# Optimization experiments

Hardware: AMD Instinct MI355X
Metric: run time of the kernel (lower is better)

Reference implementation:

```python
import jax, jax.numpy as jnp
import numpy as np

N, E = 50000, 800000
IN_DIM, HEADS, OUT_DIM = 256, 8, 32
NEG_SLOPE = 0.2  # PyG GATConv default leaky_relu slope
LN_EPS = 1e-5


def setup_inputs() -> dict:
    key = jax.random.key(0)
    ks = jax.random.split(key, 8)
    HC = HEADS * OUT_DIM
    x = jax.random.normal(ks[0], (N, IN_DIM), dtype=jnp.float32)
    edge_index = jax.random.randint(ks[1], (2, E), 0, N, dtype=jnp.int32)
    # GATConv params: lin (no bias), att_src/att_dst [H,C], output bias [H*C]
    W = jax.random.normal(ks[2], (IN_DIM, HC), dtype=jnp.float32) / np.sqrt(IN_DIM)
    att_src = jax.random.normal(ks[3], (HEADS, OUT_DIM), dtype=jnp.float32) / np.sqrt(OUT_DIM)
    att_dst = jax.random.normal(ks[4], (HEADS, OUT_DIM), dtype=jnp.float32) / np.sqrt(OUT_DIM)
    bias = jnp.zeros((HC,), dtype=jnp.float32)
    ln_gamma = jnp.ones((HC,), dtype=jnp.float32)
    ln_beta = jnp.zeros((HC,), dtype=jnp.float32)
    return {"x": x, "edge_index": edge_index, "W": W, "att_src": att_src,
            "att_dst": att_dst, "bias": bias, "ln_gamma": ln_gamma, "ln_beta": ln_beta}


def reference(x, edge_index, W, att_src, att_dst, bias, ln_gamma, ln_beta):
    n = x.shape[0]
    # GATConv adds self-loops by default
    loop = jnp.arange(n, dtype=edge_index.dtype)
    src = jnp.concatenate([edge_index[0], loop])  # [E+N]
    dst = jnp.concatenate([edge_index[1], loop])
    h = (x @ W).reshape(n, HEADS, OUT_DIM)              # [N,H,C]
    a_src = jnp.einsum('nhc,hc->nh', h, att_src)        # [N,H]
    a_dst = jnp.einsum('nhc,hc->nh', h, att_dst)
    e = jax.nn.leaky_relu(a_src[src] + a_dst[dst], NEG_SLOPE)  # [E+N,H]
    # segment-softmax over incoming edges of each destination node
    m = jax.ops.segment_max(e, dst, num_segments=n)
    e = jnp.exp(e - m[dst])
    denom = jax.ops.segment_sum(e, dst, num_segments=n)
    alpha = e / (denom[dst] + 1e-16)                    # [E+N,H]
    out = jax.ops.segment_sum(h[src] * alpha[:, :, None], dst, num_segments=n)
    out = out.reshape(n, HEADS * OUT_DIM) + bias        # concat heads + bias
    # LayerNorm(out_dim*heads); dropout is identity in eval
    mu = jnp.mean(out, axis=-1, keepdims=True)
    var = jnp.mean(jnp.square(out - mu), axis=-1, keepdims=True)
    return ln_gamma * (out - mu) * jax.lax.rsqrt(var + LN_EPS) + ln_beta
```

## Files before the change

### kernel.cpp

```cpp
#include <hip/hip_runtime.h>

#define HEADS 8
#define OUT_DIM 32
#define HC 256
#define IN_DIM 256
#define NEG_SLOPE 0.2f
#define LN_EPS 1e-5f
#define CAP 64

typedef __attribute__((ext_vector_type(8))) short bf16x8;
typedef __attribute__((ext_vector_type(4))) float f32x4;

__device__ __forceinline__ unsigned short f2bf(float f) {
    unsigned int u = __float_as_uint(f);
    unsigned int r = u + 0x7FFFu + ((u >> 16) & 1u);
    return (unsigned short)(r >> 16);
}
__device__ __forceinline__ float bf2f(unsigned short u) {
    return __uint_as_float((unsigned int)u << 16);
}

__global__ __launch_bounds__(256) void cast_wT(const float* __restrict__ W,
                                               unsigned short* __restrict__ Wt) {
    __shared__ float tile[64][65];
    const int n0 = (blockIdx.x & 3) * 64;
    const int k0 = (blockIdx.x >> 2) * 64;
    const int t = threadIdx.x;
    const int r = t >> 4;
    const int c = (t & 15) * 4;
#pragma unroll
    for (int j = 0; j < 4; j++) {
        const int kl = r + j * 16;
        const float4 v = *(const float4*)(W + (size_t)(k0 + kl) * HC + n0 + c);
        tile[kl][c + 0] = v.x; tile[kl][c + 1] = v.y;
        tile[kl][c + 2] = v.z; tile[kl][c + 3] = v.w;
    }
    __syncthreads();
#pragma unroll
    for (int j = 0; j < 4; j++) {
        const int nr = r + j * 16;
        ushort4 o;
        o.x = f2bf(tile[c + 0][nr]);
        o.y = f2bf(tile[c + 1][nr]);
        o.z = f2bf(tile[c + 2][nr]);
        o.w = f2bf(tile[c + 3][nr]);
        *(ushort4*)(Wt + (size_t)(n0 + nr) * IN_DIM + k0 + c) = o;
    }
}

__global__ __launch_bounds__(256) void gemm_bf16(const float* __restrict__ X,
                                                 const unsigned short* __restrict__ Wt,
                                                 unsigned short* __restrict__ Hb,
                                                 const float* __restrict__ att_s,
                                                 const float* __restrict__ att_d,
                                                 float* __restrict__ a_s,
                                                 float* __restrict__ a_d, int M) {
    __shared__ unsigned short smem[128 * 40 + 256 * 40];
    unsigned short* As = smem;
    unsigned short* Bs = smem + 128 * 40;
    const int t = threadIdx.x;
    const int m0 = blockIdx.x * 128;
    const int w = t >> 6, lane = t & 63;
    const int wr = w >> 1, wn = w & 1;
    const int l16 = lane & 15, quad = lane >> 4;

    f32x4 acc[4][8] = {};

    for (int k0 = 0; k0 < IN_DIM; k0 += 32) {
#pragma unroll
        for (int j = 0; j < 4; j++) {
            const int idx = t + j * 256;
            const int row = idx >> 3;
            const int part = idx & 7;
            float4 v = make_float4(0.f, 0.f, 0.f, 0.f);
            const int gm = m0 + row;
            if (gm < M) v = *(const float4*)(X + (size_t)gm * IN_DIM + k0 + part * 4);
            ushort4 b;
            b.x = f2bf(v.x); b.y = f2bf(v.y); b.z = f2bf(v.z); b.w = f2bf(v.w);
            *(ushort4*)&As[row * 40 + part * 4] = b;
        }
#pragma unroll
        for (int j = 0; j < 4; j++) {
            const int idx = t + j * 256;
            const int n = idx >> 2;
            const int part = idx & 3;
            *(uint4*)&Bs[n * 40 + part * 8] =
                *(const uint4*)(Wt + (size_t)n * IN_DIM + k0 + part * 8);
        }
        __syncthreads();

        bf16x8 af[4];
#pragma unroll
        for (int mi = 0; mi < 4; mi++) {
            const int row = wr * 64 + mi * 16 + l16;
            af[mi] = *(const bf16x8*)&As[row * 40 + quad * 8];
        }
#pragma unroll
        for (int ni = 0; ni < 8; ni++) {
            const int col = wn * 128 + ni * 16 + l16;
            const bf16x8 bfr = *(const bf16x8*)&Bs[col * 40 + quad * 8];
#pragma unroll
            for (int mi = 0; mi < 4; mi++)
                acc[mi][ni] = __builtin_amdgcn_mfma_f32_16x16x32_bf16(af[mi], bfr, acc[mi][ni], 0, 0, 0);
        }
        __syncthreads();
    }

    {
        float as_v[8], ad_v[8];
#pragma unroll
        for (int ni = 0; ni < 8; ni++) {
            as_v[ni] = att_s[wn * 128 + ni * 16 + l16];
            ad_v[ni] = att_d[wn * 128 + ni * 16 + l16];
        }
#pragma unroll
        for (int mi = 0; mi < 4; mi++) {
#pragma unroll
            for (int reg = 0; reg < 4; reg++) {
                float ps0 = acc[mi][0][reg] * as_v[0] + acc[mi][1][reg] * as_v[1];
                float ps1 = acc[mi][2][reg] * as_v[2] + acc[mi][3][reg] * as_v[3];
                float ps2 = acc[mi][4][reg] * as_v[4] + acc[mi][5][reg] * as_v[5];
                float ps3 = acc[mi][6][reg] * as_v[6] + acc[mi][7][reg] * as_v[7];
                float pd0 = acc[mi][0][reg] * ad_v[0] + acc[mi][1][reg] * ad_v[1];
                float pd1 = acc[mi][2][reg] * ad_v[2] + acc[mi][3][reg] * ad_v[3];
                float pd2 = acc[mi][4][reg] * ad_v[4] + acc[mi][5][reg] * ad_v[5];
                float pd3 = acc[mi][6][reg] * ad_v[6] + acc[mi][7][reg] * ad_v[7];
#pragma unroll
                for (int m = 1; m <= 2; m <<= 1) {
                    ps0 += __shfl_xor(ps0, m); ps1 += __shfl_xor(ps1, m);
                    ps2 += __shfl_xor(ps2, m); ps3 += __shfl_xor(ps3, m);
                    pd0 += __shfl_xor(pd0, m); pd1 += __shfl_xor(pd1, m);
                    pd2 += __shfl_xor(pd2, m); pd3 += __shfl_xor(pd3, m);
                }
                const int s2 = l16 & 3;
                float vs = s2 == 0 ? ps0 : (s2 == 1 ? ps1 : (s2 == 2 ? ps2 : ps3));
                float vd = s2 == 0 ? pd0 : (s2 == 1 ? pd1 : (s2 == 2 ? pd2 : pd3));
                vs += __shfl_xor(vs, 4); vs += __shfl_xor(vs, 8);
                vd += __shfl_xor(vd, 4); vd += __shfl_xor(vd, 8);
                const int gm = m0 + wr * 64 + mi * 16 + quad * 4 + reg;
                if (l16 < 4 && gm < M) {
                    a_s[(size_t)gm * HEADS + wn * 4 + l16] = vs;
                    a_d[(size_t)gm * HEADS + wn * 4 + l16] = vd;
                }
            }
        }
    }

    unsigned short* cbuf = smem + w * 2048;
#pragma unroll
    for (int mi = 0; mi < 4; mi++) {
#pragma unroll
        for (int ni = 0; ni < 8; ni++) {
#pragma unroll
            for (int reg = 0; reg < 4; reg++) {
                cbuf[(quad * 4 + reg) * 128 + ni * 16 + l16] = f2bf(acc[mi][ni][reg]);
            }
        }
#pragma unroll
        for (int j = 0; j < 4; j++) {
            const int q = lane + 64 * j;
            const int r = q >> 4;
            const int cc = q & 15;
            const uint4 v = *(const uint4*)&cbuf[r * 128 + cc * 8];
            const int gm = m0 + wr * 64 + mi * 16 + r;
            if (gm < M)
                *(uint4*)(Hb + (size_t)gm * HC + wn * 128 + cc * 8) = v;
        }
    }
}

__global__ __launch_bounds__(256) void bucket_scatter(const int* __restrict__ ei,
                                                      int* __restrict__ cnt,
                                                      int* __restrict__ bucket,
                                                      int E, int N) {
    const int e = blockIdx.x * 256 + threadIdx.x;
    if (e >= E + N) return;
    int s, d;
    if (e < E) { s = ei[e]; d = ei[E + e]; }
    else       { s = d = e - E; }
    int slot = atomicAdd(&cnt[d], 1);
    if (slot < CAP) bucket[(size_t)d * CAP + slot] = s;
}

__global__ __launch_bounds__(256) void csr_agg(const int* __restrict__ cntArr,
                                               const int* __restrict__ bucket,
                                               const unsigned short* __restrict__ Hb,
                                               const float* __restrict__ a_s,
                                               const float* __restrict__ a_d,
                                               const float* __restrict__ bias,
                                               const float* __restrict__ gamma,
                                               const float* __restrict__ beta,
                                               float* __restrict__ out, int N) {
    const int lane = threadIdx.x & 63;
    const int node = blockIdx.x * 4 + (threadIdx.x >> 6);
    if (node >= N) return;
    const int half = lane >> 5;
    const int sl   = lane & 31;
    const int c0   = sl * 8;
    const int hh   = sl >> 2;
    const int base = node * CAP;
    const int cnt  = min(cntArr[node], CAP);
    const float adv = a_d[(size_t)node * HEADS + hh];

    float acc[8] = {};
    float wsum = 0.f;

    for (int i = 0; i < cnt; i += 8) {
        int sv[4];
#pragma unroll
        for (int j = 0; j < 4; j++) {
            const int idx = i + 2 * j + half;
            const int sraw = bucket[base + idx];
            sv[j] = (idx < cnt) ? sraw : 0;
        }
        float tl[4];
#pragma unroll
        for (int j = 0; j < 4; j++) tl[j] = a_s[(size_t)sv[j] * HEADS + hh] + adv;
        uint4 hv[4];
#pragma unroll
        for (int j = 0; j < 4; j++) hv[j] = *(const uint4*)(Hb + (size_t)sv[j] * HC + c0);
#pragma unroll
        for (int j = 0; j < 4; j++) {
            const float l = tl[j] > 0.f ? tl[j] : NEG_SLOPE * tl[j];
            const float w = ((i + 2 * j + half) < cnt) ? __expf(l) : 0.f;
            wsum += w;
            acc[0] += w * __uint_as_float(hv[j].x << 16);
            acc[1] += w * __uint_as_float(hv[j].x & 0xffff0000u);
            acc[2] += w * __uint_as_float(hv[j].y << 16);
            acc[3] += w * __uint_as_float(hv[j].y & 0xffff0000u);
            acc[4] += w * __uint_as_float(hv[j].z << 16);
            acc[5] += w * __uint_as_float(hv[j].z & 0xffff0000u);
            acc[6] += w * __uint_as_float(hv[j].w << 16);
            acc[7] += w * __uint_as_float(hv[j].w & 0xffff0000u);
        }
    }

#pragma unroll
    for (int k = 0; k < 8; k++) acc[k] += __shfl_xor(acc[k], 32);
    wsum += __shfl_xor(wsum, 32);

    const float inv = 1.f / (wsum + 1e-16f);
    const float4 b0 = *(const float4*)(bias + c0);
    const float4 b1 = *(const float4*)(bias + c0 + 4);
    float v[8];
    v[0] = acc[0] * inv + b0.x; v[1] = acc[1] * inv + b0.y;
    v[2] = acc[2] * inv + b0.z; v[3] = acc[3] * inv + b0.w;
    v[4] = acc[4] * inv + b1.x; v[5] = acc[5] * inv + b1.y;
    v[6] = acc[6] * inv + b1.z; v[7] = acc[7] * inv + b1.w;

    float s1 = v[0] + v[1] + v[2] + v[3] + v[4] + v[5] + v[6] + v[7];
#pragma unroll
    for (int m = 1; m < 64; m <<= 1) s1 += __shfl_xor(s1, m);
    const float mu = s1 * (1.f / 512.f);
    float d[8];
    float sq = 0.f;
#pragma unroll
    for (int k = 0; k < 8; k++) { d[k] = v[k] - mu; sq += d[k] * d[k]; }
#pragma unroll
    for (int m = 1; m < 64; m <<= 1) sq += __shfl_xor(sq, m);
    const float rs = rsqrtf(sq * (1.f / 512.f) + LN_EPS);

    const float e0 = half ? d[4] : d[0];
    const float e1 = half ? d[5] : d[1];
    const float e2 = half ? d[6] : d[2];
    const float e3 = half ? d[7] : d[3];
    const int co = c0 + half * 4;
    const float4 g  = *(const float4*)(gamma + co);
    const float4 be = *(const float4*)(beta + co);
    float4 o;
    o.x = g.x * e0 * rs + be.x;
    o.y = g.y * e1 * rs + be.y;
    o.z = g.z * e2 * rs + be.z;
    o.w = g.w * e3 * rs + be.w;
    *(float4*)(out + (size_t)node * HC + co) = o;
}

extern "C" void kernel_launch(void* const* d_in, const int* in_sizes, int n_in,
                              void* d_out, int out_size, void* d_ws, size_t ws_size,
                              hipStream_t stream) {
    const float* x     = (const float*)d_in[0];
    const int*   ei    = (const int*)d_in[1];
    const float* W     = (const float*)d_in[2];
    const float* att_s = (const float*)d_in[3];
    const float* att_d = (const float*)d_in[4];
    const float* bias  = (const float*)d_in[5];
    const float* gamma = (const float*)d_in[6];
    const float* beta  = (const float*)d_in[7];
    float* out = (float*)d_out;

    const int N = in_sizes[0] / IN_DIM;
    const int E = in_sizes[1] / 2;
    const int tot = E + N;

    unsigned short* Hb = (unsigned short*)d_ws;
    unsigned short* Wt = Hb + (size_t)N * HC;
    float* a_s  = (float*)(Wt + (size_t)IN_DIM * HC);
    float* a_d  = a_s + (size_t)N * HEADS;
    int* cnt    = (int*)(a_d + (size_t)N * HEADS);
    int* bucket = cnt + N;

    hipMemsetAsync(cnt, 0, (size_t)N * sizeof(int), stream);

    bucket_scatter<<<(tot + 255) / 256, 256, 0, stream>>>(ei, cnt, bucket, E, N);
    cast_wT<<<16, 256, 0, stream>>>(W, Wt);
    gemm_bf16<<<(N + 127) / 128, 256, 0, stream>>>(x, Wt, Hb, att_s, att_d, a_s, a_d, N);

    csr_agg<<<(N + 3) / 4, 256, 0, stream>>>(cnt, bucket, Hb, a_s, a_d,
                                             bias, gamma, beta, out, N);
}
```

Baseline: 295.9 us.

## Software-pipeline neighbor gathers, preload bucket indices via shuffle, use packed fp32 FMA

The aggregation kernel now loads a node's whole bucket row (up to 64 source indices) into one register per lane and broadcasts indices with shuffles instead of issuing a global load every iteration. Gathers of a_s and the bf16 H rows for the next group of 8 edges are issued before the current group is accumulated, so memory latency overlaps with compute. Accumulation uses float2 vectors so the compiler can emit packed FMA, and leaky relu becomes fmaxf. The cost is more live registers, and the final iteration prefetches a dummy row at index 0 that is never used.

```diff
diff --git a/kernel.cpp b/kernel.cpp
--- a/kernel.cpp
+++ b/kernel.cpp
@@ -10,6 +10,7 @@
 
 typedef __attribute__((ext_vector_type(8))) short bf16x8;
 typedef __attribute__((ext_vector_type(4))) float f32x4;
+typedef __attribute__((ext_vector_type(2))) float f32x2;
 
 __device__ __forceinline__ unsigned short f2bf(float f) {
     unsigned int u = __float_as_uint(f);
@@ -201,39 +202,67 @@
     const int base = node * CAP;
     const int cnt  = min(cntArr[node], CAP);
     const float adv = a_d[(size_t)node * HEADS + hh];
-
-    float acc[8] = {};
+    const int breg = bucket[base + lane];
+
+    f32x2 acc2[4] = {};
     float wsum = 0.f;
 
-    for (int i = 0; i < cnt; i += 8) {
-        int sv[4];
-#pragma unroll
-        for (int j = 0; j < 4; j++) {
-            const int idx = i + 2 * j + half;
-            const int sraw = bucket[base + idx];
-            sv[j] = (idx < cnt) ? sraw : 0;
-        }
-        float tl[4];
-#pragma unroll
-        for (int j = 0; j < 4; j++) tl[j] = a_s[(size_t)sv[j] * HEADS + hh] + adv;
-        uint4 hv[4];
-#pragma unroll
-        for (int j = 0; j < 4; j++) hv[j] = *(const uint4*)(Hb + (size_t)sv[j] * HC + c0);
-#pragma unroll
-        for (int j = 0; j < 4; j++) {
-            const float l = tl[j] > 0.f ? tl[j] : NEG_SLOPE * tl[j];
-            const float w = ((i + 2 * j + half) < cnt) ? __expf(l) : 0.f;
+    const int nIter = (cnt + 7) >> 3;
+
+    int   sv[4];  float tl[4];  float msk[4];  uint4 hv[4];
+#pragma unroll
+    for (int j = 0; j < 4; j++) {
+        const int idx = 2 * j + half;
+        const int s = __shfl(breg, idx);
+        const bool ok = idx < cnt;
+        sv[j]  = ok ? s : 0;
+        msk[j] = ok ? 1.f : 0.f;
+    }
+#pragma unroll
+    for (int j = 0; j < 4; j++) tl[j] = a_s[(size_t)sv[j] * HEADS + hh];
+#pragma unroll
+    for (int j = 0; j < 4; j++) hv[j] = *(const uint4*)(Hb + (size_t)sv[j] * HC + c0);
+
+    for (int it = 0; it < nIter; ++it) {
+        int   sv2[4]; float tl2[4]; float msk2[4]; uint4 hv2[4];
+        const int i2 = (it + 1) * 8;
+#pragma unroll
+        for (int j = 0; j < 4; j++) {
+            const int idx = i2 + 2 * j + half;
+            const int s = __shfl(breg, idx & 63);
+            const bool ok = idx < cnt;
+            sv2[j]  = ok ? s : 0;
+            msk2[j] = ok ? 1.f : 0.f;
+        }
+#pragma unroll
+        for (int j = 0; j < 4; j++) tl2[j] = a_s[(size_t)sv2[j] * HEADS + hh];
+#pragma unroll
+        for (int j = 0; j < 4; j++) hv2[j] = *(const uint4*)(Hb + (size_t)sv2[j] * HC + c0);
+
+#pragma unroll
+        for (int j = 0; j < 4; j++) {
+            const float t = tl[j] + adv;
+            const float l = fmaxf(t, NEG_SLOPE * t);
+            const float w = msk[j] * __expf(l);
             wsum += w;
-            acc[0] += w * __uint_as_float(hv[j].x << 16);
-            acc[1] += w * __uint_as_float(hv[j].x & 0xffff0000u);
-            acc[2] += w * __uint_as_float(hv[j].y << 16);
-            acc[3] += w * __uint_as_float(hv[j].y & 0xffff0000u);
-            acc[4] += w * __uint_as_float(hv[j].z << 16);
-            acc[5] += w * __uint_as_float(hv[j].z & 0xffff0000u);
-            acc[6] += w * __uint_as_float(hv[j].w << 16);
-            acc[7] += w * __uint_as_float(hv[j].w & 0xffff0000u);
-        }
-    }
+            f32x2 wv; wv.x = w; wv.y = w;
+            f32x2 p0, p1, p2, p3;
+            p0.x = __uint_as_float(hv[j].x << 16); p0.y = __uint_as_float(hv[j].x & 0xffff0000u);
+            p1.x = __uint_as_float(hv[j].y << 16); p1.y = __uint_as_float(hv[j].y & 0xffff0000u);
+            p2.x = __uint_as_float(hv[j].z << 16); p2.y = __uint_as_float(hv[j].z & 0xffff0000u);
+            p3.x = __uint_as_float(hv[j].w << 16); p3.y = __uint_as_float(hv[j].w & 0xffff0000u);
+            acc2[0] += wv * p0;
+            acc2[1] += wv * p1;
+            acc2[2] += wv * p2;
+            acc2[3] += wv * p3;
+        }
+#pragma unroll
+        for (int j = 0; j < 4; j++) { tl[j] = tl2[j]; msk[j] = msk2[j]; hv[j] = hv2[j]; }
+    }
+
+    float acc[8];
+    acc[0] = acc2[0].x; acc[1] = acc2[0].y; acc[2] = acc2[1].x; acc[3] = acc2[1].y;
+    acc[4] = acc2[2].x; acc[5] = acc2[2].y; acc[6] = acc2[3].x; acc[7] = acc2[3].y;
 
 #pragma unroll
     for (int k = 0; k < 8; k++) acc[k] += __shfl_xor(acc[k], 32);
```

New measurement: 287.1 us. -3.0%, faster.
